# Kernel tuning notes

Measured on AMD Instinct MI355X. Metric: run time of the kernel, lower is better.

## Reference

```python
import jax, jax.numpy as jnp
import numpy as np

NUM_HEADS = 8
LATENT_FRAME = 4
D_MODEL = 1024
D_FF = 1024  # dim_feedforward == output_dim in the torch module
N_LAYERS = 6
IN_DIM = 128
LN_EPS = 1e-5


def get_slopes(n):
    # standard ALiBi slopes for power-of-two head counts: 2^{-8(i+1)/n}
    return jnp.asarray([2.0 ** (-8.0 * (i + 1) / n) for i in range(n)], jnp.float32)


def alibi_mask(num_heads, T):
    # non-causal ('future') ALiBi: additive bias -slope_h * |i - j|, shape (H, T, T)
    dist = jnp.abs(jnp.arange(T)[:, None] - jnp.arange(T)[None, :]).astype(jnp.float32)
    return -get_slopes(num_heads)[:, None, None] * dist


def layernorm(x, g, b):
    m = jnp.mean(x, axis=-1, keepdims=True)
    v = jnp.mean((x - m) ** 2, axis=-1, keepdims=True)
    return (x - m) * jax.lax.rsqrt(v + LN_EPS) * g + b


def encoder_layer(x, p, mask):
    # torch TransformerEncoderLayer, post-norm, gelu(exact), dropout=0
    B, T, D = x.shape
    H, Dh = NUM_HEADS, D // NUM_HEADS
    qkv = x @ p['in_w'].T + p['in_b']                      # (B,T,3D)
    q, k, v = jnp.split(qkv, 3, axis=-1)
    hsplit = lambda t: t.reshape(B, T, H, Dh).transpose(0, 2, 1, 3)  # (B,H,T,Dh)
    q, k, v = hsplit(q), hsplit(k), hsplit(v)
    scores = jnp.einsum('bhqd,bhkd->bhqk', q, k) / float(np.sqrt(Dh)) + mask[None]
    attn = jax.nn.softmax(scores, axis=-1)
    o = jnp.einsum('bhqk,bhkd->bhqd', attn, v).transpose(0, 2, 1, 3).reshape(B, T, D)
    o = o @ p['out_w'].T + p['out_b']
    x = layernorm(x + o, p['ln1_g'], p['ln1_b'])
    ff = jax.nn.gelu(x @ p['ff1_w'].T + p['ff1_b'], approximate=False) @ p['ff2_w'].T + p['ff2_b']
    return layernorm(x + ff, p['ln2_g'], p['ln2_b'])


def setup_inputs() -> dict:
    key = jax.random.key(0)
    ks = iter(jax.random.split(key, 32))
    s = 0.02
    B, T, F = 8, 2048, IN_DIM
    Fs = F * LATENT_FRAME  # 512
    inp = {
        'x': jax.random.normal(next(ks), (B, T, F), jnp.float32),
        'pre_w': jax.random.normal(next(ks), (D_MODEL, Fs), jnp.float32) * s,
        'pre_b': jnp.zeros((D_MODEL,), jnp.float32),
        'in_w': jax.random.normal(next(ks), (N_LAYERS, 3 * D_MODEL, D_MODEL), jnp.float32) * s,
        'in_b': jnp.zeros((N_LAYERS, 3 * D_MODEL), jnp.float32),
        'out_w': jax.random.normal(next(ks), (N_LAYERS, D_MODEL, D_MODEL), jnp.float32) * s,
        'out_b': jnp.zeros((N_LAYERS, D_MODEL), jnp.float32),
        'ln1_g': jnp.ones((N_LAYERS, D_MODEL), jnp.float32),
        'ln1_b': jnp.zeros((N_LAYERS, D_MODEL), jnp.float32),
        'ff1_w': jax.random.normal(next(ks), (N_LAYERS, D_FF, D_MODEL), jnp.float32) * s,
        'ff1_b': jnp.zeros((N_LAYERS, D_FF), jnp.float32),
        'ff2_w': jax.random.normal(next(ks), (N_LAYERS, D_MODEL, D_FF), jnp.float32) * s,
        'ff2_b': jnp.zeros((N_LAYERS, D_MODEL), jnp.float32),
        'ln2_g': jnp.ones((N_LAYERS, D_MODEL), jnp.float32),
        'ln2_b': jnp.zeros((N_LAYERS, D_MODEL), jnp.float32),
        'post_w': jax.random.normal(next(ks), (D_MODEL, D_MODEL), jnp.float32) * s,
        'post_b': jnp.zeros((D_MODEL,), jnp.float32),
    }
    return inp


def reference(x, pre_w, pre_b, in_w, in_b, out_w, out_b, ln1_g, ln1_b,
              ff1_w, ff1_b, ff2_w, ff2_b, ln2_g, ln2_b, post_w, post_b):
    B, T, F = x.shape
    Tl = T // LATENT_FRAME
    x = x.reshape(B, Tl, F * LATENT_FRAME)
    x = x @ pre_w.T + pre_b                     # (B, Tl, D)
    mask = alibi_mask(NUM_HEADS, Tl)            # (H, Tl, Tl), shared by all batches
    layers = dict(in_w=in_w, in_b=in_b, out_w=out_w, out_b=out_b,
                  ln1_g=ln1_g, ln1_b=ln1_b, ff1_w=ff1_w, ff1_b=ff1_b,
                  ff2_w=ff2_w, ff2_b=ff2_b, ln2_g=ln2_g, ln2_b=ln2_b)
    def step(h, p):
        return encoder_layer(h, p, mask), None
    x, _ = jax.lax.scan(step, x, layers)
    return x @ post_w.T + post_b
```

## Files before the change

kernel.cpp:

```cpp
#include <hip/hip_runtime.h>
#include <hip/hip_bf16.h>

#define B 8
#define TL 512
#define M_ROWS 4096
#define D 1024
#define DFF 1024
#define H 8
#define DH 128
#define NL 6

typedef unsigned short ushort_t;
typedef unsigned int uint_t;
typedef short bf16x8 __attribute__((ext_vector_type(8)));
typedef float f32x4 __attribute__((ext_vector_type(4)));

__device__ __forceinline__ ushort_t f2bf(float f) {
    uint_t u = __float_as_uint(f);
    u += 0x7FFFu + ((u >> 16) & 1u);
    return (ushort_t)(u >> 16);
}
__device__ __forceinline__ float gelu_exact(float x) {
    return 0.5f * x * (1.0f + erff(x * 0.70710678118654752f));
}
__device__ __forceinline__ void gload_lds16(const ushort_t* g, ushort_t* l) {
    __builtin_amdgcn_global_load_lds(
        (const __attribute__((address_space(1))) void*)g,
        (__attribute__((address_space(3))) void*)l, 16, 0, 0);
}
__device__ __forceinline__ void gsync_drain() {
    asm volatile("s_waitcnt vmcnt(0) lgkmcnt(0)" ::: "memory");
    __builtin_amdgcn_sched_barrier(0);
    __builtin_amdgcn_s_barrier();
}

struct CvtArgs {
    const float* s[7];
    ushort_t* d[7];
    int nq[7];
    int bstart[8];
};

__global__ __launch_bounds__(256) void cvt_all(CvtArgs a) {
    const int bid = blockIdx.x;
#pragma unroll
    for (int seg = 0; seg < 7; ++seg) {
        const int b0 = a.bstart[seg], b1 = a.bstart[seg + 1];
        if (bid < b0 || bid >= b1) continue;
        const int stride = (b1 - b0) * 256;
        const float* s = a.s[seg];
        ushort_t* d = a.d[seg];
        const int nq = a.nq[seg];
        for (int i = (bid - b0) * 256 + threadIdx.x; i < nq; i += stride) {
            float4 v = *(const float4*)(s + (size_t)i * 4);
            ushort4 o;
            o.x = f2bf(v.x); o.y = f2bf(v.y); o.z = f2bf(v.z); o.w = f2bf(v.w);
            *(ushort4*)(d + (size_t)i * 4) = o;
        }
    }
}

#define LSLOT64(r, c) (((r) * 8 + ((c) ^ ((r) & 7))) * 8)

__global__ __launch_bounds__(256) void gemm_n64(
    const ushort_t* __restrict__ A, const ushort_t* __restrict__ W,
    const float* __restrict__ bias, float* __restrict__ Cf,
    ushort_t* __restrict__ Cb, int M, int N, int K, int do_gelu) {
    __shared__ ushort_t As[2][128 * 64];
    __shared__ ushort_t Bs[2][64 * 64];

    const int tid = threadIdx.x;
    const int lane = tid & 63;
    const int w = tid >> 6;
    const int wm = (w & 2) * 32;
    const int wn = (w & 1) * 32;
    const int bm = blockIdx.y * 128;
    const int bn = blockIdx.x * 64;

    const ushort_t* gA[4];
    int sA[4];
#pragma unroll
    for (int t = 0; t < 4; ++t) {
        int s = tid + t * 256;
        int r = s >> 3, gl = (s & 7) ^ (r & 7);
        gA[t] = A + (size_t)(bm + r) * K + gl * 8;
        sA[t] = s * 8;
    }
    const ushort_t* gB[2];
    int sB[2];
#pragma unroll
    for (int t = 0; t < 2; ++t) {
        int s = tid + t * 256;
        int r = s >> 3, gl = (s & 7) ^ (r & 7);
        gB[t] = W + (size_t)(bn + r) * K + gl * 8;
        sB[t] = s * 8;
    }

    const int fr = lane & 15;
    const int fq = lane >> 4;
    int aoff[4][2], boff[2][2];
#pragma unroll
    for (int t = 0; t < 4; ++t)
#pragma unroll
        for (int s = 0; s < 2; ++s)
            aoff[t][s] = LSLOT64(wm + t * 16 + fr, s * 4 + fq);
#pragma unroll
    for (int t = 0; t < 2; ++t)
#pragma unroll
        for (int s = 0; s < 2; ++s)
            boff[t][s] = LSLOT64(wn + t * 16 + fr, s * 4 + fq);

    f32x4 acc[4][2];
#pragma unroll
    for (int i = 0; i < 4; ++i)
#pragma unroll
        for (int j = 0; j < 2; ++j) acc[i][j] = (f32x4){0.f, 0.f, 0.f, 0.f};

    auto stage = [&](int buf, int k0) {
#pragma unroll
        for (int t = 0; t < 4; ++t) gload_lds16(gA[t] + k0, &As[buf][sA[t]]);
#pragma unroll
        for (int t = 0; t < 2; ++t) gload_lds16(gB[t] + k0, &Bs[buf][sB[t]]);
    };
    auto comp = [&](int buf) {
#pragma unroll
        for (int s = 0; s < 2; ++s) {
            bf16x8 af[4], bfv[2];
#pragma unroll
            for (int t = 0; t < 4; ++t)
                af[t] = *(const bf16x8*)&As[buf][aoff[t][s]];
#pragma unroll
            for (int t = 0; t < 2; ++t)
                bfv[t] = *(const bf16x8*)&Bs[buf][boff[t][s]];
#pragma unroll
            for (int i = 0; i < 4; ++i)
#pragma unroll
                for (int j = 0; j < 2; ++j)
                    acc[i][j] = __builtin_amdgcn_mfma_f32_16x16x32_bf16(
                        af[i], bfv[j], acc[i][j], 0, 0, 0);
        }
    };

    stage(0, 0);
    gsync_drain();
    for (int k0 = 0; k0 < K; k0 += 128) {
        stage(1, k0 + 64);
        comp(0);
        gsync_drain();
        if (k0 + 128 < K) stage(0, k0 + 128);
        comp(1);
        gsync_drain();
    }

#pragma unroll
    for (int tj = 0; tj < 2; ++tj) {
        const int n = bn + wn + tj * 16 + fr;
        const float bv = bias[n];
#pragma unroll
        for (int ti = 0; ti < 4; ++ti) {
            const int m0 = bm + wm + ti * 16 + fq * 4;
            f32x4 a = acc[ti][tj];
#pragma unroll
            for (int r = 0; r < 4; ++r) {
                float v = a[r] + bv;
                if (do_gelu) v = gelu_exact(v);
                const size_t off = (size_t)(m0 + r) * N + n;
                if (Cf) Cf[off] = v;
                if (Cb) Cb[off] = f2bf(v);
            }
        }
    }
}

__global__ __launch_bounds__(256) void gemm_qkv(
    const ushort_t* __restrict__ A, const ushort_t* __restrict__ W,
    const float* __restrict__ bias, ushort_t* __restrict__ Qb,
    ushort_t* __restrict__ Kb, ushort_t* __restrict__ Vt, int K) {
    __shared__ ushort_t As[2][128 * 64];
    __shared__ ushort_t Bs[2][128 * 64];

    const int tid = threadIdx.x;
    const int lane = tid & 63;
    const int w = tid >> 6;
    const int wm = (w >> 1) * 64;
    const int wn = (w & 1) * 64;
    const int bm = blockIdx.y * 128;
    const int bn = blockIdx.x * 128;

    const ushort_t* gA[4];
    const ushort_t* gB[4];
    int sAB[4];
#pragma unroll
    for (int t = 0; t < 4; ++t) {
        int s = tid + t * 256;
        int r = s >> 3, gl = (s & 7) ^ (r & 7);
        gA[t] = A + (size_t)(bm + r) * K + gl * 8;
        gB[t] = W + (size_t)(bn + r) * K + gl * 8;
        sAB[t] = s * 8;
    }

    const int fr = lane & 15;
    const int fq = lane >> 4;
    int aoff[4][2], boff[4][2];
#pragma unroll
    for (int t = 0; t < 4; ++t)
#pragma unroll
        for (int s = 0; s < 2; ++s) {
            aoff[t][s] = LSLOT64(wm + t * 16 + fr, s * 4 + fq);
            boff[t][s] = LSLOT64(wn + t * 16 + fr, s * 4 + fq);
        }

    f32x4 acc[4][4];
#pragma unroll
    for (int i = 0; i < 4; ++i)
#pragma unroll
        for (int j = 0; j < 4; ++j) acc[i][j] = (f32x4){0.f, 0.f, 0.f, 0.f};

    auto stage = [&](int buf, int k0) {
#pragma unroll
        for (int t = 0; t < 4; ++t) gload_lds16(gA[t] + k0, &As[buf][sAB[t]]);
#pragma unroll
        for (int t = 0; t < 4; ++t) gload_lds16(gB[t] + k0, &Bs[buf][sAB[t]]);
    };
    auto comp = [&](int buf) {
#pragma unroll
        for (int s = 0; s < 2; ++s) {
            bf16x8 af[4], bfv[4];
#pragma unroll
            for (int t = 0; t < 4; ++t)
                af[t] = *(const bf16x8*)&As[buf][aoff[t][s]];
#pragma unroll
            for (int t = 0; t < 4; ++t)
                bfv[t] = *(const bf16x8*)&Bs[buf][boff[t][s]];
#pragma unroll
            for (int i = 0; i < 4; ++i)
#pragma unroll
                for (int j = 0; j < 4; ++j)
                    acc[i][j] = __builtin_amdgcn_mfma_f32_16x16x32_bf16(
                        af[i], bfv[j], acc[i][j], 0, 0, 0);
        }
    };

    stage(0, 0);
    gsync_drain();
    for (int k0 = 0; k0 < K; k0 += 128) {
        stage(1, k0 + 64);
        comp(0);
        gsync_drain();
        if (k0 + 128 < K) stage(0, k0 + 128);
        comp(1);
        gsync_drain();
    }

    const float qscale = 0.08838834764831845f;
#pragma unroll
    for (int tj = 0; tj < 4; ++tj) {
        const int n = bn + wn + tj * 16 + fr;
        const float bv = bias[n];
#pragma unroll
        for (int ti = 0; ti < 4; ++ti) {
            const int m0 = bm + wm + ti * 16 + fq * 4;
            f32x4 a = acc[ti][tj];
            if (n < D) {
#pragma unroll
                for (int r = 0; r < 4; ++r)
                    Qb[(size_t)(m0 + r) * D + n] = f2bf((a[r] + bv) * qscale);
            } else if (n < 2 * D) {
#pragma unroll
                for (int r = 0; r < 4; ++r)
                    Kb[(size_t)(m0 + r) * D + (n - D)] = f2bf(a[r] + bv);
            } else {
                const int h = (n - 2 * D) >> 7;
                const int dh = (n - 2 * D) & 127;
                const int bb = m0 >> 9;
                const int t = m0 & 511;
                ushort4 pk;
                pk.x = f2bf(a[0] + bv); pk.y = f2bf(a[1] + bv);
                pk.z = f2bf(a[2] + bv); pk.w = f2bf(a[3] + bv);
                *(ushort4*)&Vt[((size_t)(bb * H + h) * DH + dh) * TL + t] = pk;
            }
        }
    }
}

#define LSW16(r, g) ((((r) << 4) + ((g) ^ ((r) & 7))) << 3)
#define LSW8(r, g) ((((r) << 3) + ((g) ^ ((r) & 7))) << 3)

__global__ __launch_bounds__(256, 2) void attn_mfma(
    const ushort_t* __restrict__ Qb, const ushort_t* __restrict__ Kb,
    const ushort_t* __restrict__ Vt, ushort_t* __restrict__ Ab) {
    __shared__ ushort_t Qs[64 * 128];
    __shared__ ushort_t Ks[64 * 128];
    __shared__ ushort_t Vts[128 * 64];
    __shared__ ushort_t Ps[64 * 72];

    const int q0 = blockIdx.x * 64;
    const int bh = blockIdx.y;
    const int b = bh >> 3;
    const int h = bh & 7;
    const int tid = threadIdx.x;
    const int lane = tid & 63;
    const int w = tid >> 6;
    const int fr = lane & 15;
    const int fq = lane >> 4;

    const float slope = exp2f(-(float)(h + 1));

#pragma unroll
    for (int kk = 0; kk < 4; ++kk) {
        int s = tid + kk * 256;
        int r = s >> 4, gp = s & 15, gl = gp ^ (r & 7);
        gload_lds16(Qb + (size_t)(b * TL + q0 + r) * D + h * DH + gl * 8,
                    &Qs[s * 8]);
    }

    f32x4 o8[8];
    float m_i[4], l_i[4];
#pragma unroll
    for (int nt = 0; nt < 8; ++nt) o8[nt] = (f32x4){0.f, 0.f, 0.f, 0.f};
#pragma unroll
    for (int r = 0; r < 4; ++r) { m_i[r] = -1e30f; l_i[r] = 0.f; }

    for (int kt = 0; kt < TL / 64; ++kt) {
        __syncthreads();
#pragma unroll
        for (int kk = 0; kk < 4; ++kk) {
            int s = tid + kk * 256;
            int r = s >> 4, gp = s & 15, gl = gp ^ (r & 7);
            gload_lds16(Kb + (size_t)(b * TL + kt * 64 + r) * D + h * DH + gl * 8,
                        &Ks[s * 8]);
        }
#pragma unroll
        for (int kk = 0; kk < 4; ++kk) {
            int s = tid + kk * 256;
            int r = s >> 3, gp = s & 7, gl = gp ^ (r & 7);
            gload_lds16(Vt + ((size_t)bh * DH + r) * TL + kt * 64 + gl * 8,
                        &Vts[s * 8]);
        }
        __syncthreads();

        f32x4 sacc[4];
#pragma unroll
        for (int jt = 0; jt < 4; ++jt) sacc[jt] = (f32x4){0.f, 0.f, 0.f, 0.f};
#pragma unroll
        for (int s4 = 0; s4 < 4; ++s4) {
            bf16x8 aq = *(const bf16x8*)&Qs[LSW16(w * 16 + fr, s4 * 4 + fq)];
#pragma unroll
            for (int jt = 0; jt < 4; ++jt) {
                bf16x8 kb = *(const bf16x8*)&Ks[LSW16(jt * 16 + fr, s4 * 4 + fq)];
                sacc[jt] = __builtin_amdgcn_mfma_f32_16x16x32_bf16(
                    aq, kb, sacc[jt], 0, 0, 0);
            }
        }

        const int iq = q0 + w * 16 + fq * 4;
        const int jk = kt * 64 + fr;
        float al[4];
#pragma unroll
        for (int r = 0; r < 4; ++r) {
            float sv[4];
#pragma unroll
            for (int jt = 0; jt < 4; ++jt)
                sv[jt] = sacc[jt][r] -
                         slope * fabsf((float)(iq + r - jk - jt * 16));
            float mx = fmaxf(fmaxf(sv[0], sv[1]), fmaxf(sv[2], sv[3]));
            mx = fmaxf(mx, __shfl_xor(mx, 1));
            mx = fmaxf(mx, __shfl_xor(mx, 2));
            mx = fmaxf(mx, __shfl_xor(mx, 4));
            mx = fmaxf(mx, __shfl_xor(mx, 8));
            float mnew = fmaxf(m_i[r], mx);
            al[r] = __expf(m_i[r] - mnew);
            float rs = 0.f;
#pragma unroll
            for (int jt = 0; jt < 4; ++jt) {
                sv[jt] = __expf(sv[jt] - mnew);
                rs += sv[jt];
            }
            rs += __shfl_xor(rs, 1);
            rs += __shfl_xor(rs, 2);
            rs += __shfl_xor(rs, 4);
            rs += __shfl_xor(rs, 8);
            l_i[r] = l_i[r] * al[r] + rs;
            m_i[r] = mnew;
            const int prow = w * 16 + fq * 4 + r;
#pragma unroll
            for (int jt = 0; jt < 4; ++jt)
                Ps[prow * 72 + jt * 16 + fr] = f2bf(sv[jt]);
        }
#pragma unroll
        for (int nt = 0; nt < 8; ++nt)
#pragma unroll
            for (int r = 0; r < 4; ++r) o8[nt][r] *= al[r];

#pragma unroll
        for (int s2 = 0; s2 < 2; ++s2) {
            bf16x8 pa = *(const bf16x8*)&Ps[(w * 16 + fr) * 72 + s2 * 32 + fq * 8];
#pragma unroll
            for (int nt = 0; nt < 8; ++nt) {
                bf16x8 vb = *(const bf16x8*)&Vts[LSW8(nt * 16 + fr, s2 * 4 + fq)];
                o8[nt] = __builtin_amdgcn_mfma_f32_16x16x32_bf16(
                    pa, vb, o8[nt], 0, 0, 0);
            }
        }
    }

#pragma unroll
    for (int r = 0; r < 4; ++r) {
        float inv = 1.f / l_i[r];
        const size_t base = (size_t)(b * TL + q0 + w * 16 + fq * 4 + r) * D + h * DH;
#pragma unroll
        for (int nt = 0; nt < 8; ++nt)
            Ab[base + nt * 16 + fr] = f2bf(o8[nt][r] * inv);
    }
}

__global__ __launch_bounds__(256) void add_ln(const float* __restrict__ x,
                                              const float* __restrict__ y,
                                              const float* __restrict__ g,
                                              const float* __restrict__ bta,
                                              float* __restrict__ out,
                                              ushort_t* __restrict__ outb) {
    const int row = blockIdx.x * 4 + (threadIdx.x >> 6);
    const int lane = threadIdx.x & 63;
    const size_t rbase = (size_t)row * D;

    float4 v[4];
#pragma unroll
    for (int j = 0; j < 4; ++j) {
        float4 xv = *(const float4*)(x + rbase + lane * 4 + j * 256);
        float4 yv = *(const float4*)(y + rbase + lane * 4 + j * 256);
        v[j].x = xv.x + yv.x; v[j].y = xv.y + yv.y;
        v[j].z = xv.z + yv.z; v[j].w = xv.w + yv.w;
    }

    float s = 0.f;
#pragma unroll
    for (int j = 0; j < 4; ++j) s += v[j].x + v[j].y + v[j].z + v[j].w;
#pragma unroll
    for (int off = 32; off; off >>= 1) s += __shfl_xor(s, off);
    const float mean = s * (1.f / (float)D);

    float sq = 0.f;
#pragma unroll
    for (int j = 0; j < 4; ++j) {
        float d0 = v[j].x - mean, d1 = v[j].y - mean;
        float d2 = v[j].z - mean, d3 = v[j].w - mean;
        sq += d0 * d0 + d1 * d1 + d2 * d2 + d3 * d3;
    }
#pragma unroll
    for (int off = 32; off; off >>= 1) sq += __shfl_xor(sq, off);
    const float var = sq * (1.f / (float)D);
    const float inv = rsqrtf(var + 1e-5f);

#pragma unroll
    for (int j = 0; j < 4; ++j) {
        const int col = lane * 4 + j * 256;
        float4 gv = *(const float4*)(g + col);
        float4 bv = *(const float4*)(bta + col);
        float4 o;
        o.x = (v[j].x - mean) * inv * gv.x + bv.x;
        o.y = (v[j].y - mean) * inv * gv.y + bv.y;
        o.z = (v[j].z - mean) * inv * gv.z + bv.z;
        o.w = (v[j].w - mean) * inv * gv.w + bv.w;
        *(float4*)(out + rbase + col) = o;
        ushort4 ob;
        ob.x = f2bf(o.x); ob.y = f2bf(o.y); ob.z = f2bf(o.z); ob.w = f2bf(o.w);
        *(ushort4*)(outb + rbase + col) = ob;
    }
}

extern "C" void kernel_launch(void* const* d_in, const int* in_sizes, int n_in,
                              void* d_out, int out_size, void* d_ws, size_t ws_size,
                              hipStream_t stream) {
    const float* x_in   = (const float*)d_in[0];
    const float* pre_w  = (const float*)d_in[1];
    const float* pre_b  = (const float*)d_in[2];
    const float* in_w   = (const float*)d_in[3];
    const float* in_b   = (const float*)d_in[4];
    const float* out_w  = (const float*)d_in[5];
    const float* out_b  = (const float*)d_in[6];
    const float* ln1_g  = (const float*)d_in[7];
    const float* ln1_b  = (const float*)d_in[8];
    const float* ff1_w  = (const float*)d_in[9];
    const float* ff1_b  = (const float*)d_in[10];
    const float* ff2_w  = (const float*)d_in[11];
    const float* ff2_b  = (const float*)d_in[12];
    const float* ln2_g  = (const float*)d_in[13];
    const float* ln2_b  = (const float*)d_in[14];
    const float* post_w = (const float*)d_in[15];
    const float* post_b = (const float*)d_in[16];

    float* X = (float*)d_ws;
    float* Y = X + (size_t)M_ROWS * D;
    ushort_t* Xb   = (ushort_t*)(Y + (size_t)M_ROWS * D);
    ushort_t* Ab   = Xb + (size_t)M_ROWS * D;
    ushort_t* Qb   = Ab + (size_t)M_ROWS * D;
    ushort_t* Kb   = Qb + (size_t)M_ROWS * D;
    ushort_t* Vt   = Kb + (size_t)M_ROWS * D;
    ushort_t* xinb = Vt + (size_t)M_ROWS * D;
    ushort_t* pwb  = xinb + (size_t)M_ROWS * 512;
    ushort_t* iwb  = pwb + (size_t)D * 512;
    ushort_t* owb  = iwb + (size_t)NL * 3 * D * D;
    ushort_t* f1wb = owb + (size_t)NL * D * D;
    ushort_t* f2wb = f1wb + (size_t)NL * DFF * D;
    ushort_t* powb = f2wb + (size_t)NL * D * DFF;

    const dim3 blk(256);

    CvtArgs ca;
    ca.s[0] = x_in;   ca.d[0] = xinb; ca.nq[0] = (M_ROWS * 512) / 4;
    ca.s[1] = pre_w;  ca.d[1] = pwb;  ca.nq[1] = (D * 512) / 4;
    ca.s[2] = in_w;   ca.d[2] = iwb;  ca.nq[2] = (NL * 3 * D * D) / 4;
    ca.s[3] = out_w;  ca.d[3] = owb;  ca.nq[3] = (NL * D * D) / 4;
    ca.s[4] = ff1_w;  ca.d[4] = f1wb; ca.nq[4] = (NL * DFF * D) / 4;
    ca.s[5] = ff2_w;  ca.d[5] = f2wb; ca.nq[5] = (NL * D * DFF) / 4;
    ca.s[6] = post_w; ca.d[6] = powb; ca.nq[6] = (D * D) / 4;
    {
        long long total = 0;
        for (int i = 0; i < 7; ++i) total += ca.nq[i];
        long long cum = 0;
        ca.bstart[0] = 0;
        for (int i = 0; i < 7; ++i) {
            cum += ca.nq[i];
            ca.bstart[i + 1] = (int)((cum * 4096) / total);
        }
        ca.bstart[7] = 4096;
    }
    cvt_all<<<4096, blk, 0, stream>>>(ca);

    const dim3 gN64(D / 64, M_ROWS / 128);
    const dim3 gQKV(3 * D / 128, M_ROWS / 128);

    gemm_n64<<<gN64, blk, 0, stream>>>(xinb, pwb, pre_b, X, Xb,
                                       M_ROWS, D, 512, 0);

    for (int l = 0; l < NL; ++l) {
        gemm_qkv<<<gQKV, blk, 0, stream>>>(Xb, iwb + (size_t)l * 3 * D * D,
                                           in_b + (size_t)l * 3 * D,
                                           Qb, Kb, Vt, D);
        attn_mfma<<<dim3(TL / 64, B * H), blk, 0, stream>>>(Qb, Kb, Vt, Ab);
        gemm_n64<<<gN64, blk, 0, stream>>>(Ab, owb + (size_t)l * D * D,
                                           out_b + (size_t)l * D, Y, nullptr,
                                           M_ROWS, D, D, 0);
        add_ln<<<dim3(M_ROWS / 4), blk, 0, stream>>>(X, Y, ln1_g + (size_t)l * D,
                                                     ln1_b + (size_t)l * D, X, Xb);
        gemm_n64<<<gN64, blk, 0, stream>>>(Xb, f1wb + (size_t)l * DFF * D,
                                           ff1_b + (size_t)l * DFF, nullptr, Ab,
                                           M_ROWS, DFF, D, 1);
        gemm_n64<<<gN64, blk, 0, stream>>>(Ab, f2wb + (size_t)l * D * DFF,
                                           ff2_b + (size_t)l * D, Y, nullptr,
                                           M_ROWS, D, DFF, 0);
        add_ln<<<dim3(M_ROWS / 4), blk, 0, stream>>>(X, Y, ln2_g + (size_t)l * D,
                                                     ln2_b + (size_t)l * D, X, Xb);
    }

    gemm_n64<<<gN64, blk, 0, stream>>>(Xb, powb, post_b, (float*)d_out, nullptr,
                                       M_ROWS, D, D, 0);
}
```

Baseline: 1.289 ms.

## Replace QKV GEMM with 256x256 tile, 8-wave pipelined kernel; simplify n64 GEMM

```diff
diff --git a/kernel.cpp b/kernel.cpp
--- a/kernel.cpp
+++ b/kernel.cpp
@@ -27,11 +27,6 @@
     __builtin_amdgcn_global_load_lds(
         (const __attribute__((address_space(1))) void*)g,
         (__attribute__((address_space(3))) void*)l, 16, 0, 0);
-}
-__device__ __forceinline__ void gsync_drain() {
-    asm volatile("s_waitcnt vmcnt(0) lgkmcnt(0)" ::: "memory");
-    __builtin_amdgcn_sched_barrier(0);
-    __builtin_amdgcn_s_barrier();
 }
 
 struct CvtArgs {
@@ -66,8 +61,8 @@
     const ushort_t* __restrict__ A, const ushort_t* __restrict__ W,
     const float* __restrict__ bias, float* __restrict__ Cf,
     ushort_t* __restrict__ Cb, int M, int N, int K, int do_gelu) {
-    __shared__ ushort_t As[2][128 * 64];
-    __shared__ ushort_t Bs[2][64 * 64];
+    __shared__ ushort_t As[128 * 64];
+    __shared__ ushort_t Bs[64 * 64];
 
     const int tid = threadIdx.x;
     const int lane = tid & 63;
@@ -78,22 +73,22 @@
     const int bn = blockIdx.x * 64;
 
     const ushort_t* gA[4];
-    int sA[4];
+    ushort_t* lA[4];
 #pragma unroll
     for (int t = 0; t < 4; ++t) {
         int s = tid + t * 256;
         int r = s >> 3, gl = (s & 7) ^ (r & 7);
         gA[t] = A + (size_t)(bm + r) * K + gl * 8;
-        sA[t] = s * 8;
+        lA[t] = &As[s * 8];
     }
     const ushort_t* gB[2];
-    int sB[2];
+    ushort_t* lB[2];
 #pragma unroll
     for (int t = 0; t < 2; ++t) {
         int s = tid + t * 256;
         int r = s >> 3, gl = (s & 7) ^ (r & 7);
         gB[t] = W + (size_t)(bn + r) * K + gl * 8;
-        sB[t] = s * 8;
+        lB[t] = &Bs[s * 8];
     }
 
     const int fr = lane & 15;
@@ -116,40 +111,28 @@
 #pragma unroll
         for (int j = 0; j < 2; ++j) acc[i][j] = (f32x4){0.f, 0.f, 0.f, 0.f};
 
-    auto stage = [&](int buf, int k0) {
-#pragma unroll
-        for (int t = 0; t < 4; ++t) gload_lds16(gA[t] + k0, &As[buf][sA[t]]);
-#pragma unroll
-        for (int t = 0; t < 2; ++t) gload_lds16(gB[t] + k0, &Bs[buf][sB[t]]);
-    };
-    auto comp = [&](int buf) {
+    for (int k0 = 0; k0 < K; k0 += 64) {
+#pragma unroll
+        for (int t = 0; t < 4; ++t) gload_lds16(gA[t] + k0, lA[t]);
+#pragma unroll
+        for (int t = 0; t < 2; ++t) gload_lds16(gB[t] + k0, lB[t]);
+        __syncthreads();
+
 #pragma unroll
         for (int s = 0; s < 2; ++s) {
-            bf16x8 af[4], bfv[2];
-#pragma unroll
-            for (int t = 0; t < 4; ++t)
-                af[t] = *(const bf16x8*)&As[buf][aoff[t][s]];
-#pragma unroll
-            for (int t = 0; t < 2; ++t)
-                bfv[t] = *(const bf16x8*)&Bs[buf][boff[t][s]];
+            bf16x8 af[4], bf[2];
+#pragma unroll
+            for (int t = 0; t < 4; ++t) af[t] = *(const bf16x8*)&As[aoff[t][s]];
+#pragma unroll
+            for (int t = 0; t < 2; ++t) bf[t] = *(const bf16x8*)&Bs[boff[t][s]];
 #pragma unroll
             for (int i = 0; i < 4; ++i)
 #pragma unroll
                 for (int j = 0; j < 2; ++j)
                     acc[i][j] = __builtin_amdgcn_mfma_f32_16x16x32_bf16(
-                        af[i], bfv[j], acc[i][j], 0, 0, 0);
-        }
-    };
-
-    stage(0, 0);
-    gsync_drain();
-    for (int k0 = 0; k0 < K; k0 += 128) {
-        stage(1, k0 + 64);
-        comp(0);
-        gsync_drain();
-        if (k0 + 128 < K) stage(0, k0 + 128);
-        comp(1);
-        gsync_drain();
+                        af[i], bf[j], acc[i][j], 0, 0, 0);
+        }
+        __syncthreads();
     }
 
 #pragma unroll
@@ -172,95 +155,129 @@
     }
 }
 
-__global__ __launch_bounds__(256) void gemm_qkv(
+#define QPHASE(par, mh, nh, LOADA, ...)                                        \
+    {                                                                          \
+        if (LOADA) {                                                           \
+            _Pragma("unroll") for (int im = 0; im < 4; ++im)                   \
+                _Pragma("unroll") for (int ks = 0; ks < 2; ++ks)               \
+                    af[im][ks] = *(const bf16x8*)&AsB[(par)*16384 +            \
+                                                     (mh)*8192 + aoff[im][ks]];\
+        }                                                                      \
+        _Pragma("unroll") for (int jn = 0; jn < 2; ++jn)                       \
+            _Pragma("unroll") for (int ks = 0; ks < 2; ++ks)                   \
+                bfv[jn][ks] = *(const bf16x8*)&BsB[(par)*16384 +               \
+                                                  (nh)*8192 + boff[jn][ks]];   \
+        __VA_ARGS__;                                                           \
+        __builtin_amdgcn_s_barrier();                                          \
+        asm volatile("s_waitcnt lgkmcnt(0)" ::: "memory");                     \
+        __builtin_amdgcn_sched_barrier(0);                                     \
+        __builtin_amdgcn_s_setprio(1);                                         \
+        _Pragma("unroll") for (int im = 0; im < 4; ++im)                       \
+            _Pragma("unroll") for (int jn = 0; jn < 2; ++jn)                   \
+                _Pragma("unroll") for (int ks = 0; ks < 2; ++ks)               \
+                    acc[(mh)*4 + im][(nh)*2 + jn] =                            \
+                        __builtin_amdgcn_mfma_f32_16x16x32_bf16(               \
+                            af[im][ks], bfv[jn][ks],                           \
+                            acc[(mh)*4 + im][(nh)*2 + jn], 0, 0, 0);           \
+        __builtin_amdgcn_s_setprio(0);                                         \
+        asm volatile("s_waitcnt vmcnt(4)" ::: "memory");                       \
+        __builtin_amdgcn_s_barrier();                                          \
+    }
+
+__global__ __launch_bounds__(512, 2) void gemm_qkv256(
     const ushort_t* __restrict__ A, const ushort_t* __restrict__ W,
     const float* __restrict__ bias, ushort_t* __restrict__ Qb,
-    ushort_t* __restrict__ Kb, ushort_t* __restrict__ Vt, int K) {
-    __shared__ ushort_t As[2][128 * 64];
-    __shared__ ushort_t Bs[2][128 * 64];
+    ushort_t* __restrict__ Kb, ushort_t* __restrict__ Vt) {
+    extern __shared__ ushort_t lds[];
+    ushort_t* AsB = lds;
+    ushort_t* BsB = lds + 32768;
+    const int K = 1024;
+
+    const int bid = blockIdx.x;
+    const int wg = (bid & 7) * 24 + (bid >> 3);
+    const int by = wg / 12, bx = wg - by * 12;
+    const int bm = by * 256, bn = bx * 256;
 
     const int tid = threadIdx.x;
     const int lane = tid & 63;
     const int w = tid >> 6;
-    const int wm = (w >> 1) * 64;
-    const int wn = (w & 1) * 64;
-    const int bm = blockIdx.y * 128;
-    const int bn = blockIdx.x * 128;
-
-    const ushort_t* gA[4];
-    const ushort_t* gB[4];
-    int sAB[4];
-#pragma unroll
-    for (int t = 0; t < 4; ++t) {
-        int s = tid + t * 256;
-        int r = s >> 3, gl = (s & 7) ^ (r & 7);
-        gA[t] = A + (size_t)(bm + r) * K + gl * 8;
-        gB[t] = W + (size_t)(bn + r) * K + gl * 8;
-        sAB[t] = s * 8;
-    }
-
+    const int wm = w >> 2;
+    const int wn = w & 3;
     const int fr = lane & 15;
     const int fq = lane >> 4;
-    int aoff[4][2], boff[4][2];
-#pragma unroll
-    for (int t = 0; t < 4; ++t)
-#pragma unroll
-        for (int s = 0; s < 2; ++s) {
-            aoff[t][s] = LSLOT64(wm + t * 16 + fr, s * 4 + fq);
-            boff[t][s] = LSLOT64(wn + t * 16 + fr, s * 4 + fq);
-        }
-
-    f32x4 acc[4][4];
-#pragma unroll
-    for (int i = 0; i < 4; ++i)
+
+    const ushort_t* gA[2];
+    const ushort_t* gB[2];
+    int sdst[2];
+#pragma unroll
+    for (int u = 0; u < 2; ++u) {
+        int s = tid + u * 512;
+        int r = s >> 3, c = (s & 7) ^ (r & 7);
+        gA[u] = A + (size_t)(bm + r) * K + c * 8;
+        gB[u] = W + (size_t)(bn + r) * K + c * 8;
+        sdst[u] = s * 8;
+    }
+
+    int aoff[4][2], boff[2][2];
+#pragma unroll
+    for (int im = 0; im < 4; ++im)
+#pragma unroll
+        for (int ks = 0; ks < 2; ++ks)
+            aoff[im][ks] = LSLOT64(wm * 64 + im * 16 + fr, ks * 4 + fq);
+#pragma unroll
+    for (int jn = 0; jn < 2; ++jn)
+#pragma unroll
+        for (int ks = 0; ks < 2; ++ks)
+            boff[jn][ks] = LSLOT64(wn * 32 + jn * 16 + fr, ks * 4 + fq);
+
+    f32x4 acc[8][4];
+#pragma unroll
+    for (int i = 0; i < 8; ++i)
 #pragma unroll
         for (int j = 0; j < 4; ++j) acc[i][j] = (f32x4){0.f, 0.f, 0.f, 0.f};
 
-    auto stage = [&](int buf, int k0) {
-#pragma unroll
-        for (int t = 0; t < 4; ++t) gload_lds16(gA[t] + k0, &As[buf][sAB[t]]);
-#pragma unroll
-        for (int t = 0; t < 4; ++t) gload_lds16(gB[t] + k0, &Bs[buf][sAB[t]]);
+    auto stageA = [&](int p, int h, int tk) {
+#pragma unroll
+        for (int u = 0; u < 2; ++u)
+            gload_lds16(gA[u] + (size_t)h * 128 * K + tk * 64,
+                        &AsB[p * 16384 + h * 8192 + sdst[u]]);
     };
-    auto comp = [&](int buf) {
-#pragma unroll
-        for (int s = 0; s < 2; ++s) {
-            bf16x8 af[4], bfv[4];
-#pragma unroll
-            for (int t = 0; t < 4; ++t)
-                af[t] = *(const bf16x8*)&As[buf][aoff[t][s]];
-#pragma unroll
-            for (int t = 0; t < 4; ++t)
-                bfv[t] = *(const bf16x8*)&Bs[buf][boff[t][s]];
-#pragma unroll
-            for (int i = 0; i < 4; ++i)
-#pragma unroll
-                for (int j = 0; j < 4; ++j)
-                    acc[i][j] = __builtin_amdgcn_mfma_f32_16x16x32_bf16(
-                        af[i], bfv[j], acc[i][j], 0, 0, 0);
-        }
+    auto stageB = [&](int p, int h, int tk) {
+#pragma unroll
+        for (int u = 0; u < 2; ++u)
+            gload_lds16(gB[u] + (size_t)h * 128 * K + tk * 64,
+                        &BsB[p * 16384 + h * 8192 + sdst[u]]);
     };
 
-    stage(0, 0);
-    gsync_drain();
-    for (int k0 = 0; k0 < K; k0 += 128) {
-        stage(1, k0 + 64);
-        comp(0);
-        gsync_drain();
-        if (k0 + 128 < K) stage(0, k0 + 128);
-        comp(1);
-        gsync_drain();
+    stageA(0, 0, 0); stageB(0, 0, 0); stageB(0, 1, 0); stageA(0, 1, 0);
+    asm volatile("s_waitcnt vmcnt(0)" ::: "memory");
+    __builtin_amdgcn_s_barrier();
+
+    bf16x8 af[4][2], bfv[2][2];
+
+#pragma unroll 1
+    for (int it = 0; it < 8; ++it) {
+        const int t0 = 2 * it;
+        QPHASE(0, 0, 0, 1, { stageA(1, 0, t0 + 1); })
+        QPHASE(0, 0, 1, 0, { stageB(1, 0, t0 + 1); })
+        QPHASE(0, 1, 0, 1, { stageB(1, 1, t0 + 1); })
+        QPHASE(0, 1, 1, 0, { stageA(1, 1, t0 + 1); })
+        const bool st = (it < 7);
+        QPHASE(1, 0, 0, 1, { if (st) stageA(0, 0, t0 + 2); })
+        QPHASE(1, 0, 1, 0, { if (st) stageB(0, 0, t0 + 2); })
+        QPHASE(1, 1, 0, 1, { if (st) stageB(0, 1, t0 + 2); })
+        QPHASE(1, 1, 1, 0, { if (st) stageA(0, 1, t0 + 2); })
     }
 
     const float qscale = 0.08838834764831845f;
 #pragma unroll
-    for (int tj = 0; tj < 4; ++tj) {
-        const int n = bn + wn + tj * 16 + fr;
+    for (int j = 0; j < 4; ++j) {
+        const int n = bn + (j >> 1) * 128 + wn * 32 + (j & 1) * 16 + fr;
         const float bv = bias[n];
 #pragma unroll
-        for (int ti = 0; ti < 4; ++ti) {
-            const int m0 = bm + wm + ti * 16 + fq * 4;
-            f32x4 a = acc[ti][tj];
+        for (int i = 0; i < 8; ++i) {
+            const int m0 = bm + (i >> 2) * 128 + wm * 64 + (i & 3) * 16 + fq * 4;
+            f32x4 a = acc[i][j];
             if (n < D) {
 #pragma unroll
                 for (int r = 0; r < 4; ++r)
@@ -490,6 +507,13 @@
     const float* post_w = (const float*)d_in[15];
     const float* post_b = (const float*)d_in[16];
 
+    static bool attr_set = false;
+    if (!attr_set) {
+        hipFuncSetAttribute((const void*)gemm_qkv256,
+                            hipFuncAttributeMaxDynamicSharedMemorySize, 131072);
+        attr_set = true;
+    }
+
     float* X = (float*)d_ws;
     float* Y = X + (size_t)M_ROWS * D;
     ushort_t* Xb   = (ushort_t*)(Y + (size_t)M_ROWS * D);
@@ -529,15 +553,14 @@
     cvt_all<<<4096, blk, 0, stream>>>(ca);
 
     const dim3 gN64(D / 64, M_ROWS / 128);
-    const dim3 gQKV(3 * D / 128, M_ROWS / 128);
 
     gemm_n64<<<gN64, blk, 0, stream>>>(xinb, pwb, pre_b, X, Xb,
                                        M_ROWS, D, 512, 0);
 
     for (int l = 0; l < NL; ++l) {
-        gemm_qkv<<<gQKV, blk, 0, stream>>>(Xb, iwb + (size_t)l * 3 * D * D,
-                                           in_b + (size_t)l * 3 * D,
-                                           Qb, Kb, Vt, D);
+        gemm_qkv256<<<dim3(192), dim3(512), 131072, stream>>>(
+            Xb, iwb + (size_t)l * 3 * D * D, in_b + (size_t)l * 3 * D,
+            Qb, Kb, Vt);
         attn_mfma<<<dim3(TL / 64, B * H), blk, 0, stream>>>(Qb, Kb, Vt, Ab);
         gemm_n64<<<gN64, blk, 0, stream>>>(Ab, owb + (size_t)l * D * D,
                                            out_b + (size_t)l * D, Y, nullptr,
```

Result: faster. 1.131 ms (-12.2%).
